# Performance work log

Hardware: AMD Instinct MI355X
Metric: run time of the kernel (lower is better)

Reference implementation:

```python
import jax, jax.numpy as jnp
import numpy as np

N_HEAD = 12
D_MODEL = 768
B, T = 1, 1024


def _rope(x):
    # x: (B, H, T, Dh). Matches torch RoPE: split even/odd, cat halves.
    Dh = x.shape[-1]
    t = x.shape[2]
    inv_freq = 1.0 / (10000.0 ** (jnp.arange(0, Dh, 2, dtype=jnp.float32) / Dh))
    freqs = jnp.arange(t, dtype=jnp.float32)[:, None] * inv_freq[None, :]  # (T, Dh/2)
    cos = jnp.cos(freqs)[None, None]  # (1,1,T,Dh/2)
    sin = jnp.sin(freqs)[None, None]
    x1 = x[..., 0::2]
    x2 = x[..., 1::2]
    return jnp.concatenate([-x2 * sin + x1 * cos, x1 * sin + x2 * cos], axis=-1)


def _wedge(x, A, id_bias):
    # S = (A - A^T) + diag(id_bias_h), per head h; x: (B,H,T,Dh)
    skew = A - A.T  # (Dh, Dh)
    S = skew[None, :, :] + jax.vmap(jnp.diag)(id_bias)  # (H, Dh, Dh)
    flow = jnp.einsum('bhtd,hde->bhte', x, S)
    return x + flow


def _forward(x, WV_w, WV_b, WK_w, WK_b, WQ_w, A, id_bias, sink, v_nulls, WO_w, WO_b):
    b, t, c = x.shape
    n_br = WO_w.shape[0]
    n_sh = n_br
    dh = c // n_br
    h_tot = n_br * n_sh
    scale = dh ** -0.5

    q = (x @ WQ_w).reshape(b, t, h_tot, dh).transpose(0, 2, 1, 3)      # (B,Htot,T,Dh)
    k_base = (x @ WK_w + WK_b).reshape(b, t, n_sh, dh).transpose(0, 2, 1, 3)
    v_base = (x @ WV_w + WV_b).reshape(b, t, n_sh, dh).transpose(0, 2, 1, 3)
    k = jnp.tile(k_base, (1, n_br, 1, 1))  # (B,Htot,T,Dh)
    v = jnp.tile(v_base, (1, n_br, 1, 1))

    q = _rope(_wedge(q, A, id_bias))
    k = _rope(_wedge(k, A, id_bias))

    scores = jnp.einsum('bhtd,bhsd->bhts', q, k) * scale  # (B,Htot,T,T)
    causal = jnp.tril(jnp.ones((t, t), dtype=bool))
    scores = jnp.where(causal[None, None], scores, -jnp.inf)

    sinks = jnp.broadcast_to(sink.reshape(1, h_tot, 1, 1), (b, h_tot, t, 1))
    probs = jax.nn.softmax(jnp.concatenate([scores, sinks], axis=-1), axis=-1)
    probs_tok, probs_sink = probs[..., :t], probs[..., t:]

    out_tok = jnp.einsum('bhts,bhsd->bhtd', probs_tok, v)
    out_sink = probs_sink * v_nulls.reshape(h_tot, dh)[None, :, None, :]
    ctx = out_tok + out_sink  # (B,Htot,T,Dh)

    ctx = ctx.reshape(b, n_br, n_sh, t, dh).transpose(0, 1, 3, 2, 4).reshape(b, n_br, t, c)
    y = jnp.einsum('bntc,ncd->bntd', ctx, WO_w) + WO_b[None, :, None, :]
    return y.mean(axis=1)  # (B,T,C)


def setup_inputs() -> dict:
    key = jax.random.key(0)
    ks = jax.random.split(key, 12)
    c = D_MODEL
    n_br = N_HEAD
    dh = c // n_br
    h_tot = n_br * n_br
    s = 0.02
    return {
        'x': jax.random.normal(ks[0], (B, T, c), dtype=jnp.float32),
        'WV_w': jax.random.normal(ks[1], (c, c), dtype=jnp.float32) * s,
        'WV_b': jnp.zeros((c,), dtype=jnp.float32),
        'WK_w': jax.random.normal(ks[2], (c, c), dtype=jnp.float32) * s,
        'WK_b': jnp.zeros((c,), dtype=jnp.float32),
        'WQ_w': jax.random.normal(ks[3], (c, c * n_br), dtype=jnp.float32) * s,
        'A': jax.random.normal(ks[4], (dh, dh), dtype=jnp.float32) * s,
        'id_bias': jax.random.normal(ks[5], (h_tot, dh), dtype=jnp.float32) * s,
        'sink': jax.random.normal(ks[6], (h_tot,), dtype=jnp.float32) * s,
        'v_nulls': jax.random.normal(ks[7], (n_br, c), dtype=jnp.float32) * s,
        'WO_w': jax.random.normal(ks[8], (n_br, c, c), dtype=jnp.float32) * (1.0 / np.sqrt(c)),
        'WO_b': jnp.zeros((n_br, c), dtype=jnp.float32),
    }


def reference(x, WV_w, WV_b, WK_w, WK_b, WQ_w, A, id_bias, sink, v_nulls, WO_w, WO_b):
    return _forward(x, WV_w, WV_b, WK_w, WK_b, WQ_w, A, id_bias, sink, v_nulls, WO_w, WO_b)
```

## Files before the change

### kernel.cpp

```cpp
#include <hip/hip_runtime.h>
#include <hip/hip_bf16.h>

#define T_SEQ   1024
#define C_MODEL 768
#define N_BR    12
#define DH      64
#define H_TOT   144
#define NQ      9216

typedef __bf16 bf16x8 __attribute__((ext_vector_type(8)));
typedef float  f32x4  __attribute__((ext_vector_type(4)));
typedef unsigned int u32x4 __attribute__((ext_vector_type(4)));
typedef unsigned short u16;

#define SM_OFF 3.0f

__device__ __forceinline__ void gload16(void* lds, const void* g)
{
    __builtin_amdgcn_global_load_lds(
        (const __attribute__((address_space(1))) void*)g,
        (__attribute__((address_space(3))) void*)lds, 16, 0, 0);
}

__device__ __forceinline__ void split1(float x, u16& h, u16& l)
{
    __bf16 bh = (__bf16)x;
    __bf16 bl = (__bf16)(x - (float)bh);
    h = __builtin_bit_cast(u16, bh);
    l = __builtin_bit_cast(u16, bl);
}

__device__ __forceinline__ u16 tobf(float x)
{
    return __builtin_bit_cast(u16, (__bf16)x);
}

__device__ __forceinline__ unsigned cvtpk(float a, float b)
{
    unsigned r;
    asm("v_cvt_pk_bf16_f32 %0, %1, %2" : "=v"(r) : "v"(a), "v"(b));
    return r;
}

__device__ __forceinline__ int swb(int row, int byteoff)
{
    return row * 128 + (byteoff ^ ((row & 7) << 4));
}

__device__ __forceinline__ bf16x8 ldsr8(const u16* p, int byteoff)
{
    return *reinterpret_cast<const bf16x8*>(reinterpret_cast<const char*>(p) + byteoff);
}

__device__ __forceinline__ void convt_body(const float* __restrict__ W,
                                           u16* __restrict__ out, int K, int N,
                                           int nx, int ky, float (*t)[33], int tid)
{
    const int n0 = nx * 32;
    const int k0 = ky * 32;
    const int tx = tid & 31;
    const int ty = tid >> 5;
    #pragma unroll
    for (int r = 0; r < 4; ++r)
        t[ty + r * 8][tx] = W[(size_t)(k0 + ty + r * 8) * N + n0 + tx];
    __syncthreads();
    #pragma unroll
    for (int r = 0; r < 4; ++r)
        out[(size_t)(n0 + ty + r * 8) * K + k0 + tx] = tobf(t[tx][ty + r * 8]);
}

__global__ __launch_bounds__(256)
void prep_kernel(const float* __restrict__ x, u16* __restrict__ xh,
                 const float* __restrict__ Amat, const float* __restrict__ id_bias,
                 u16* __restrict__ Mth, u16* __restrict__ Mtl,
                 const float* __restrict__ WO_b, float* __restrict__ mbias,
                 float* __restrict__ tab,
                 const float* __restrict__ WO_w, u16* __restrict__ wot,
                 const float* __restrict__ WK_w, const float* __restrict__ WV_w,
                 u16* __restrict__ wkvt)
{
    __shared__ float tsh[32][33];
    const int b   = blockIdx.x;
    const int tid = threadIdx.x;

    if (b < 128) {
        const int idx = b * 256 + tid;
        const int t = idx >> 5, i = idx & 31;
        const float inv = expf(-(float)i * (logf(10000.f) / 32.f));
        const float fr = (float)t * inv;
        tab[t * 64 + i]      = cosf(fr);
        tab[t * 64 + 32 + i] = sinf(fr);
    } else if (b < 272) {
        const int h = b - 128;
        const int base = tid * 16;
        #pragma unroll
        for (int i = 0; i < 16; ++i) {
            const int idx = base + i;
            const int e = idx >> 6, d = idx & 63;
            float v = Amat[d * 64 + e] - Amat[e * 64 + d];
            if (d == e) v += 1.0f + id_bias[h * 64 + d];
            u16 hh, ll;
            split1(v, hh, ll);
            Mth[(size_t)h * 4096 + idx] = hh;
            Mtl[(size_t)h * 4096 + idx] = ll;
        }
    } else if (b < 275) {
        const int d = (b - 272) * 256 + tid;
        if (d < C_MODEL) {
            float s = 0.f;
            #pragma unroll
            for (int n = 0; n < N_BR; ++n) s += WO_b[n * C_MODEL + d];
            mbias[d] = s * (1.0f / 12.0f);
        }
    } else if (b < 1043) {
        const size_t i = (size_t)(b - 275) * 1024 + tid * 4;
        float4 v = *reinterpret_cast<const float4*>(&x[i]);
        ushort4 o = { tobf(v.x), tobf(v.y), tobf(v.z), tobf(v.w) };
        *reinterpret_cast<ushort4*>(&xh[i]) = o;
    } else if (b < 7955) {
        const int u = b - 1043;
        convt_body(WO_w, wot, NQ, C_MODEL, u % 24, u / 24, tsh, tid);
    } else if (b < 8531) {
        const int u = b - 7955;
        convt_body(WK_w, wkvt, C_MODEL, C_MODEL, u % 24, u / 24, tsh, tid);
    } else {
        const int u = b - 8531;
        convt_body(WV_w, wkvt + 589824, C_MODEL, C_MODEL, u % 24, u / 24, tsh, tid);
    }
}

#define BM 128
#define BN 128
#define BK 32

__global__ __launch_bounds__(256)
void gemm_bf16_kernel(const u16* __restrict__ A, const u16* __restrict__ B,
                      float* __restrict__ Cp, int M, int N, int K)
{
    __shared__ __align__(16) u16 sA[BM * BK], sB[BN * BK];

    const int tid  = threadIdx.x;
    const int lane = tid & 63;
    const int wid  = tid >> 6;
    const int m0   = blockIdx.y * BM;
    const int n0   = blockIdx.x * BN;
    const int kc   = K / gridDim.z;
    const int kbeg = blockIdx.z * kc;
    const int kend = kbeg + kc;

    const int wm = (wid >> 1) * 64;
    const int wn = (wid & 1) * 64;

    f32x4 acc[4][4];
    #pragma unroll
    for (int i = 0; i < 4; ++i)
        #pragma unroll
        for (int j = 0; j < 4; ++j)
            #pragma unroll
            for (int r = 0; r < 4; ++r) acc[i][j][r] = 0.f;

    const int r0 = tid >> 2;
    const int c0 = tid & 3;
    const int rA = wm + (lane & 15);
    const int rB = wn + (lane & 15);
    const int co = (lane >> 4) * 8;

    for (int k0 = kbeg; k0 < kend; k0 += BK) {
        gload16(&sA[(size_t)tid * 8],         &A[(size_t)(m0 + r0)      * K + k0 + c0 * 8]);
        gload16(&sA[(size_t)(tid + 256) * 8], &A[(size_t)(m0 + r0 + 64) * K + k0 + c0 * 8]);
        gload16(&sB[(size_t)tid * 8],         &B[(size_t)(n0 + r0)      * K + k0 + c0 * 8]);
        gload16(&sB[(size_t)(tid + 256) * 8], &B[(size_t)(n0 + r0 + 64) * K + k0 + c0 * 8]);
        __syncthreads();

        bf16x8 ah[4], bh[4];
        #pragma unroll
        for (int i = 0; i < 4; ++i)
            ah[i] = *reinterpret_cast<const bf16x8*>(&sA[(size_t)(rA + i * 16) * BK + co]);
        #pragma unroll
        for (int j = 0; j < 4; ++j)
            bh[j] = *reinterpret_cast<const bf16x8*>(&sB[(size_t)(rB + j * 16) * BK + co]);
        #pragma unroll
        for (int i = 0; i < 4; ++i)
            #pragma unroll
            for (int j = 0; j < 4; ++j)
                acc[i][j] = __builtin_amdgcn_mfma_f32_16x16x32_bf16(ah[i], bh[j], acc[i][j], 0, 0, 0);
        __syncthreads();
    }

    float* Cz = Cp + (size_t)blockIdx.z * M * N;
    const int crow0 = m0 + wm + (lane >> 4) * 4;
    const int ccol0 = n0 + wn + (lane & 15);
    #pragma unroll
    for (int i = 0; i < 4; ++i)
        #pragma unroll
        for (int j = 0; j < 4; ++j)
            #pragma unroll
            for (int r = 0; r < 4; ++r)
                Cz[(size_t)(crow0 + i * 16 + r) * N + ccol0 + j * 16] = acc[i][j][r];
}

__global__ __launch_bounds__(256)
void gemm64_kernel(const u16* __restrict__ A, const u16* __restrict__ B,
                   float* __restrict__ Cp, int M, int N, int K)
{
    __shared__ __align__(16) u16 sA[64 * BK], sB[128 * BK];

    const int tid  = threadIdx.x;
    const int lane = tid & 63;
    const int wid  = tid >> 6;
    const int m0   = blockIdx.y * 64;
    const int n0   = blockIdx.x * 128;
    const int kc   = K / gridDim.z;
    const int kbeg = blockIdx.z * kc;
    const int kend = kbeg + kc;

    const int wm = (wid >> 1) * 32;
    const int wn = (wid & 1) * 64;
    const int g  = lane >> 4;
    const int li = lane & 15;

    f32x4 acc[2][4];
    #pragma unroll
    for (int i = 0; i < 2; ++i)
        #pragma unroll
        for (int j = 0; j < 4; ++j)
            #pragma unroll
            for (int r = 0; r < 4; ++r) acc[i][j][r] = 0.f;

    const int r0 = tid >> 2;
    const int c0 = (tid & 3) * 8;

    for (int k0 = kbeg; k0 < kend; k0 += BK) {
        gload16(&sA[(size_t)tid * 8],         &A[(size_t)(m0 + r0)      * K + k0 + c0]);
        gload16(&sB[(size_t)tid * 8],         &B[(size_t)(n0 + r0)      * K + k0 + c0]);
        gload16(&sB[(size_t)(tid + 256) * 8], &B[(size_t)(n0 + r0 + 64) * K + k0 + c0]);
        __syncthreads();

        bf16x8 ah[2], bh[4];
        #pragma unroll
        for (int i = 0; i < 2; ++i)
            ah[i] = *reinterpret_cast<const bf16x8*>(&sA[(size_t)(wm + 16 * i + li) * BK + g * 8]);
        #pragma unroll
        for (int j = 0; j < 4; ++j)
            bh[j] = *reinterpret_cast<const bf16x8*>(&sB[(size_t)(wn + 16 * j + li) * BK + g * 8]);
        #pragma unroll
        for (int i = 0; i < 2; ++i)
            #pragma unroll
            for (int j = 0; j < 4; ++j)
                acc[i][j] = __builtin_amdgcn_mfma_f32_16x16x32_bf16(ah[i], bh[j], acc[i][j], 0, 0, 0);
        __syncthreads();
    }

    float* Cz = Cp + (size_t)blockIdx.z * M * N;
    const int crow0 = m0 + wm + g * 4;
    const int ccol0 = n0 + wn + li;
    #pragma unroll
    for (int i = 0; i < 2; ++i)
        #pragma unroll
        for (int j = 0; j < 4; ++j)
            #pragma unroll
            for (int r = 0; r < 4; ++r)
                Cz[(size_t)(crow0 + i * 16 + r) * N + ccol0 + j * 16] = acc[i][j][r];
}

__global__ __launch_bounds__(256)
void gemm_q_rope_kernel(const u16* __restrict__ A, const u16* __restrict__ B,
                        const float* __restrict__ tab, u16* __restrict__ Q2)
{
    __shared__ __align__(16) u16 sA[64 * BK], sB[128 * BK];

    const int K = C_MODEL;
    const int tid  = threadIdx.x;
    const int lane = tid & 63;
    const int wid  = tid >> 6;
    const int m0   = blockIdx.y * 64;
    const int n0   = blockIdx.x * 128;

    const int wm = (wid >> 1) * 32;
    const int wn = (wid & 1) * 64;
    const int g  = lane >> 4;
    const int li = lane & 15;

    f32x4 acc[2][4];
    #pragma unroll
    for (int i = 0; i < 2; ++i)
        #pragma unroll
        for (int j = 0; j < 4; ++j)
            #pragma unroll
            for (int r = 0; r < 4; ++r) acc[i][j][r] = 0.f;

    const int r0 = tid >> 2;
    const int c0 = (tid & 3) * 8;

    for (int k0 = 0; k0 < K; k0 += BK) {
        gload16(&sA[(size_t)tid * 8],         &A[(size_t)(m0 + r0)      * K + k0 + c0]);
        gload16(&sB[(size_t)tid * 8],         &B[(size_t)(n0 + r0)      * K + k0 + c0]);
        gload16(&sB[(size_t)(tid + 256) * 8], &B[(size_t)(n0 + r0 + 64) * K + k0 + c0]);
        __syncthreads();

        bf16x8 ah[2], bh[4];
        #pragma unroll
        for (int i = 0; i < 2; ++i)
            ah[i] = *reinterpret_cast<const bf16x8*>(&sA[(size_t)(wm + 16 * i + li) * BK + g * 8]);
        #pragma unroll
        for (int j = 0; j < 4; ++j)
            bh[j] = *reinterpret_cast<const bf16x8*>(&sB[(size_t)(wn + 16 * j + li) * BK + g * 8]);
        #pragma unroll
        for (int i = 0; i < 2; ++i)
            #pragma unroll
            for (int j = 0; j < 4; ++j)
                acc[i][j] = __builtin_amdgcn_mfma_f32_16x16x32_bf16(ah[i], bh[j], acc[i][j], 0, 0, 0);
        __syncthreads();
    }

    const int h  = (n0 + wn) >> 6;
    const bool ev = (li & 1) == 0;
    #pragma unroll
    for (int j = 0; j < 4; ++j) {
        const int e  = j * 16 + li;
        const int i2 = e >> 1;
        #pragma unroll
        for (int i = 0; i < 2; ++i) {
            #pragma unroll
            for (int r = 0; r < 4; ++r) {
                const int t = m0 + wm + i * 16 + g * 4 + r;
                const float own = acc[i][j][r];
                const float oth = __shfl_xor(own, 1);
                const float cs = tab[t * 64 + i2];
                const float sn = tab[t * 64 + 32 + i2];
                float o; int ch;
                if (ev) { o = own * cs - oth * sn; ch = i2; }
                else    { o = oth * sn + own * cs; ch = 32 + i2; }
                Q2[((size_t)h * T_SEQ + t) * 64 + ch] = tobf(o * 0.125f);
            }
        }
    }
}

__global__ __launch_bounds__(256)
void reduce_kernel(const float* __restrict__ part, float* __restrict__ out,
                   const float* __restrict__ bias, int MN, int N, int Z, float alpha)
{
    const int i = (blockIdx.x * 256 + threadIdx.x) * 4;
    if (i >= MN) return;
    float4 s = *reinterpret_cast<const float4*>(&part[i]);
    for (int z = 1; z < Z; ++z) {
        float4 p = *reinterpret_cast<const float4*>(&part[(size_t)z * MN + i]);
        s.x += p.x; s.y += p.y; s.z += p.z; s.w += p.w;
    }
    s.x *= alpha; s.y *= alpha; s.z *= alpha; s.w *= alpha;
    if (bias) {
        const int c = i % N;
        s.x += bias[c]; s.y += bias[c + 1]; s.z += bias[c + 2]; s.w += bias[c + 3];
    }
    *reinterpret_cast<float4*>(&out[i]) = s;
}

__global__ __launch_bounds__(256)
void reduce_kv_kernel(const float* __restrict__ part, float* __restrict__ out,
                      const float* __restrict__ kb, const float* __restrict__ vb,
                      int MN, int Z)
{
    const int i = (blockIdx.x * 256 + threadIdx.x) * 4;
    if (i >= MN) return;
    float4 s = *reinterpret_cast<const float4*>(&part[i]);
    for (int z = 1; z < Z; ++z) {
        float4 p = *reinterpret_cast<const float4*>(&part[(size_t)z * MN + i]);
        s.x += p.x; s.y += p.y; s.z += p.z; s.w += p.w;
    }
    const int c = i % 1536;
    const float* bp = (c < 768) ? (kb + c) : (vb + c - 768);
    s.x += bp[0]; s.y += bp[1]; s.z += bp[2]; s.w += bp[3];
    *reinterpret_cast<float4*>(&out[i]) = s;
}

__global__ __launch_bounds__(256)
void fold_wq_kernel(const float* __restrict__ WQ, const u16* __restrict__ Mth,
                    const u16* __restrict__ Mtl, u16* __restrict__ wqt)
{
    __shared__ __align__(16) u16 sMh[4096], sMl[4096];
    __shared__ __align__(16) u16 sB[8192];

    const int h   = blockIdx.x;
    const int k0  = blockIdx.y * 128;
    const int tid = threadIdx.x;
    const int lane = tid & 63, w = tid >> 6, g = lane >> 4, li = lane & 15;

    {
        const char* gmh = (const char*)(Mth + (size_t)h * 4096);
        const char* gml = (const char*)(Mtl + (size_t)h * 4096);
        #pragma unroll
        for (int p = 0; p < 2; ++p) {
            const int u = p * 256 + tid;
            const int row = u >> 3, off = (u & 7) * 16;
            const int src = swb(row, off);
            gload16((char*)sMh + u * 16, gmh + src);
            gload16((char*)sMl + u * 16, gml + src);
        }
    }
    {
        const int r    = tid >> 1;
        const int half = tid & 1;
        const float* src = WQ + (size_t)(k0 + r) * NQ + h * 64 + half * 32;
        #pragma unroll
        for (int q = 0; q < 8; ++q) {
            float4 v = *reinterpret_cast<const float4*>(&src[q * 4]);
            ushort4 o = { tobf(v.x), tobf(v.y), tobf(v.z), tobf(v.w) };
            const int byte = swb(r, half * 64 + q * 8);
            *reinterpret_cast<ushort4*>(reinterpret_cast<char*>(sB) + byte) = o;
        }
    }
    __syncthreads();

    f32x4 acc[4][2];
    #pragma unroll
    for (int i = 0; i < 4; ++i)
        #pragma unroll
        for (int jj = 0; jj < 2; ++jj)
            #pragma unroll
            for (int r = 0; r < 4; ++r) acc[i][jj][r] = 0.f;

    bf16x8 ah[4][2], al[4][2];
    #pragma unroll
    for (int i = 0; i < 4; ++i)
        #pragma unroll
        for (int ks = 0; ks < 2; ++ks) {
            ah[i][ks] = ldsr8(sMh, swb(16 * i + li, ks * 64 + g * 16));
            al[i][ks] = ldsr8(sMl, swb(16 * i + li, ks * 64 + g * 16));
        }
    #pragma unroll
    for (int jj = 0; jj < 2; ++jj) {
        const int brow = 16 * (2 * w + jj) + li;
        #pragma unroll
        for (int ks = 0; ks < 2; ++ks) {
            bf16x8 bh = ldsr8(sB, swb(brow, ks * 64 + g * 16));
            #pragma unroll
            for (int i = 0; i < 4; ++i) {
                acc[i][jj] = __builtin_amdgcn_mfma_f32_16x16x32_bf16(ah[i][ks], bh, acc[i][jj], 0, 0, 0);
                acc[i][jj] = __builtin_amdgcn_mfma_f32_16x16x32_bf16(al[i][ks], bh, acc[i][jj], 0, 0, 0);
            }
        }
    }

    #pragma unroll
    for (int i = 0; i < 4; ++i)
        #pragma unroll
        for (int jj = 0; jj < 2; ++jj) {
            const int kc = k0 + 16 * (2 * w + jj) + li;
            #pragma unroll
            for (int r = 0; r < 4; ++r) {
                const int e = 16 * i + g * 4 + r;
                wqt[((size_t)h * 64 + e) * 768 + kc] = tobf(acc[i][jj][r]);
            }
        }
}

__global__ __launch_bounds__(256)
void wedge_mfma_kernel(const float* __restrict__ X, u16* __restrict__ Y,
                       const u16* __restrict__ Mth, const u16* __restrict__ Mtl,
                       const float* __restrict__ tab, int inStride, int headMod)
{
    const int h   = blockIdx.x;
    const int t0  = blockIdx.y * 64;
    const int tid = threadIdx.x;
    const int lane = tid & 63;
    const int w    = tid >> 6;
    const int g    = lane >> 4;
    const int li   = lane & 15;

    __shared__ __align__(16) u16 sX[4096], sMh[4096], sMl[4096];

    {
        const int r  = tid >> 2;
        const int c0 = (tid & 3) * 16;
        const float* xrow = X + (size_t)(t0 + r) * inStride + (h % headMod) * 64;
        #pragma unroll
        for (int q = 0; q < 4; ++q) {
            const int c = c0 + q * 4;
            float4 v = *reinterpret_cast<const float4*>(&xrow[c]);
            ushort4 hv = { tobf(v.x), tobf(v.y), tobf(v.z), tobf(v.w) };
            *reinterpret_cast<ushort4*>(reinterpret_cast<char*>(sX) + swb(r, 2 * c)) = hv;
        }
    }
    {
        const char* gmh = (const char*)(Mth + (size_t)h * 4096);
        const char* gml = (const char*)(Mtl + (size_t)h * 4096);
        #pragma unroll
        for (int u = 0; u < 2; ++u) {
            const int L = (u * 256 + tid) * 16;
            const int row = L >> 7, off = L & 127;
            const int src = swb(row, off);
            gload16(reinterpret_cast<char*>(sMh) + L, gmh + src);
            gload16(reinterpret_cast<char*>(sMl) + L, gml + src);
        }
    }
    __syncthreads();

    f32x4 acc[4];
    #pragma unroll
    for (int j = 0; j < 4; ++j)
        #pragma unroll
        for (int r = 0; r < 4; ++r) acc[j][r] = 0.f;

    bf16x8 ah[2];
    #pragma unroll
    for (int ks = 0; ks < 2; ++ks)
        ah[ks] = ldsr8(sX, swb(w * 16 + li, ks * 64 + g * 16));
    #pragma unroll
    for (int ks = 0; ks < 2; ++ks)
        #pragma unroll
        for (int j = 0; j < 4; ++j) {
            bf16x8 bh = ldsr8(sMh, swb(16 * j + li, ks * 64 + g * 16));
            bf16x8 bl = ldsr8(sMl, swb(16 * j + li, ks * 64 + g * 16));
            acc[j] = __builtin_amdgcn_mfma_f32_16x16x32_bf16(ah[ks], bh, acc[j], 0, 0, 0);
            acc[j] = __builtin_amdgcn_mfma_f32_16x16x32_bf16(ah[ks], bl, acc[j], 0, 0, 0);
        }

    const bool ev = (li & 1) == 0;
    #pragma unroll
    for (int j = 0; j < 4; ++j) {
        const int e = 16 * j + li;
        const int i2 = e >> 1;
        #pragma unroll
        for (int r = 0; r < 4; ++r) {
            const int t = t0 + w * 16 + g * 4 + r;
            const float own = acc[j][r];
            const float oth = __shfl_xor(own, 1);
            const float cs = tab[t * 64 + i2];
            const float sn = tab[t * 64 + 32 + i2];
            float o; int ch;
            if (ev) { o = own * cs - oth * sn; ch = i2; }
            else    { o = oth * sn + own * cs; ch = 32 + i2; }
            Y[((size_t)h * T_SEQ + t) * 64 + ch] = tobf(o);
        }
    }
}

__global__ __launch_bounds__(256)
void vt_kernel(const float* __restrict__ vb, u16* __restrict__ Vt, int stride)
{
    __shared__ float Ls[64][65];
    const int s  = blockIdx.x;
    const int t0 = blockIdx.y * 64;
    const int tid = threadIdx.x;
    {
        const int r  = tid >> 2;
        const int c0 = (tid & 3) * 16;
        const float* row = vb + (size_t)(t0 + r) * stride + s * 64;
        #pragma unroll
        for (int q = 0; q < 4; ++q) {
            float4 v = *reinterpret_cast<const float4*>(&row[c0 + q * 4]);
            Ls[r][c0 + q * 4 + 0] = v.x; Ls[r][c0 + q * 4 + 1] = v.y;
            Ls[r][c0 + q * 4 + 2] = v.z; Ls[r][c0 + q * 4 + 3] = v.w;
        }
    }
    __syncthreads();
    {
        const int d  = tid >> 2;
        const int tq = (tid & 3) * 16;
        u16* orow = Vt + ((size_t)s * 64 + d) * T_SEQ + t0 + tq;
        #pragma unroll
        for (int q = 0; q < 4; ++q) {
            ushort4 o;
            o.x = tobf(Ls[tq + q * 4 + 0][d]);
            o.y = tobf(Ls[tq + q * 4 + 1][d]);
            o.z = tobf(Ls[tq + q * 4 + 2][d]);
            o.w = tobf(Ls[tq + q * 4 + 3][d]);
            *reinterpret_cast<ushort4*>(&orow[q * 4]) = o;
        }
    }
}

__device__ __forceinline__ void attn_stage_kv(
    int buf, int kv0, int h, int s, int tid,
    const u16* __restrict__ K2, const u16* __restrict__ Vt,
    u16* sK, u16* sV)
{
    const char* gk = (const char*)(K2 + ((size_t)h * T_SEQ + kv0) * 64);
    const char* gv = (const char*)Vt + (size_t)s * 131072 + kv0 * 2;
    #pragma unroll
    for (int p = 0; p < 2; ++p) {
        const int u = p * 256 + tid;
        const int row = u >> 3;
        const int off = (u & 7) * 16;
        const int sw  = off ^ ((row & 7) << 4);
        const int j  = row >> 4, g2 = (row >> 2) & 3, rr = row & 3;
        const int srow = 32 * (j & 1) + 8 * g2 + 4 * (j >> 1) + rr;
        gload16((char*)sK + buf * 8192 + u * 16, gk + srow * 128 + sw);
        gload16((char*)sV + buf * 8192 + u * 16, gv + row * 2048 + sw);
    }
}

template<bool DIAG>
__device__ __forceinline__ void attn_tile_sw(
    int kv0, int qglob, int g, int li,
    const u16* sK, const u16* sV, const bf16x8* qa,
    f32x4* acc, float& psum)
{
    f32x4 sacc[4];
    #pragma unroll
    for (int j = 0; j < 4; ++j)
        #pragma unroll
        for (int r = 0; r < 4; ++r) sacc[j][r] = 0.f;

    __builtin_amdgcn_s_setprio(1);
    #pragma unroll
    for (int ks = 0; ks < 2; ++ks)
        #pragma unroll
        for (int j = 0; j < 4; ++j) {
            bf16x8 kb = ldsr8(sK, swb(16 * j + li, ks * 64 + g * 16));
            sacc[j] = __builtin_amdgcn_mfma_f32_16x16x32_bf16(kb, qa[ks], sacc[j], 0, 0, 0);
        }
    __builtin_amdgcn_s_setprio(0);

    float p[4][4];
    const int kvb = kv0 + 8 * g;
    #pragma unroll
    for (int j = 0; j < 4; ++j)
        #pragma unroll
        for (int r = 0; r < 4; ++r) {
            float sv_ = sacc[j][r];
            if (DIAG) {
                const int kv = kvb + 32 * (j & 1) + 4 * (j >> 1) + r;
                if (kv > qglob) sv_ = -__builtin_inff();
            }
            p[j][r] = __expf(sv_ - SM_OFF);
        }
    psum += ((p[0][0] + p[0][1]) + (p[0][2] + p[0][3]))
          + ((p[1][0] + p[1][1]) + (p[1][2] + p[1][3]))
          + ((p[2][0] + p[2][1]) + (p[2][2] + p[2][3]))
          + ((p[3][0] + p[3][1]) + (p[3][2] + p[3][3]));

    __builtin_amdgcn_s_setprio(1);
    #pragma unroll
    for (int ks = 0; ks < 2; ++ks) {
        u32x4 pw;
        pw[0] = cvtpk(p[ks][0],     p[ks][1]);
        pw[1] = cvtpk(p[ks][2],     p[ks][3]);
        pw[2] = cvtpk(p[ks + 2][0], p[ks + 2][1]);
        pw[3] = cvtpk(p[ks + 2][2], p[ks + 2][3]);
        bf16x8 pa = __builtin_bit_cast(bf16x8, pw);
        #pragma unroll
        for (int j = 0; j < 4; ++j) {
            bf16x8 vb = ldsr8(sV, swb(16 * j + li, ks * 64 + g * 16));
            acc[j] = __builtin_amdgcn_mfma_f32_16x16x32_bf16(vb, pa, acc[j], 0, 0, 0);
        }
    }
    __builtin_amdgcn_s_setprio(0);
}

__global__ __launch_bounds__(256)
void attn_mfma_kernel(const u16* __restrict__ Q2, const u16* __restrict__ K2,
                      const u16* __restrict__ Vt, const float* __restrict__ sink,
                      const float* __restrict__ v_nulls, u16* __restrict__ ctxb)
{
    const int h  = blockIdx.x;
    const int qt = 15 - (int)blockIdx.y;
    const int s  = h % N_BR;
    const int tid  = threadIdx.x;
    const int lane = tid & 63, w = tid >> 6, g = lane >> 4, li = lane & 15;

    __shared__ __align__(16) u16 sQ[4096];
    __shared__ __align__(16) u16 sK[8192];
    __shared__ __align__(16) u16 sV[8192];

    {
        const char* gq = (const char*)(Q2 + ((size_t)h * T_SEQ + qt * 64) * 64);
        #pragma unroll
        for (int p = 0; p < 2; ++p) {
            const int u = p * 256 + tid;
            const int row = u >> 3, off = (u & 7) * 16;
            gload16((char*)sQ + u * 16, gq + row * 128 + (off ^ ((row & 7) << 4)));
        }
    }
    attn_stage_kv(0, 0, h, s, tid, K2, Vt, sK, sV);
    __syncthreads();

    bf16x8 qa[2];
    #pragma unroll
    for (int ks = 0; ks < 2; ++ks)
        qa[ks] = ldsr8(sQ, swb(w * 16 + li, ks * 64 + g * 16));

    f32x4 acc[4];
    #pragma unroll
    for (int j = 0; j < 4; ++j)
        #pragma unroll
        for (int r = 0; r < 4; ++r) acc[j][r] = 0.f;
    float psum = 0.f;

    const int qglob = qt * 64 + w * 16 + li;
    const int nt = qt + 1;
    int cur = 0;
    for (int kt = 0; kt < nt - 1; ++kt) {
        attn_stage_kv(cur ^ 1, (kt + 1) * 64, h, s, tid, K2, Vt, sK, sV);
        attn_tile_sw<false>(kt * 64, qglob, g, li,
                            sK + cur * 4096, sV + cur * 4096, qa, acc, psum);
        __syncthreads();
        cur ^= 1;
    }
    attn_tile_sw<true>(qt * 64, qglob, g, li,
                       sK + cur * 4096, sV + cur * 4096, qa, acc, psum);

    psum += __shfl_xor(psum, 16);
    psum += __shfl_xor(psum, 32);
    const float es = __expf(sink[h] - SM_OFF);
    const float rz = 1.0f / (psum + es);

    const int t = qt * 64 + w * 16 + li;
    u16* orow = ctxb + (size_t)t * NQ + h * 64;
    const float* vn = v_nulls + h * 64;
    #pragma unroll
    for (int j = 0; j < 4; ++j) {
        const int d0 = 16 * j + 4 * g;
        float4 vnv = *reinterpret_cast<const float4*>(&vn[d0]);
        ushort4 o;
        o.x = tobf((acc[j][0] + es * vnv.x) * rz);
        o.y = tobf((acc[j][1] + es * vnv.y) * rz);
        o.z = tobf((acc[j][2] + es * vnv.z) * rz);
        o.w = tobf((acc[j][3] + es * vnv.w) * rz);
        *reinterpret_cast<ushort4*>(&orow[d0]) = o;
    }
}

extern "C" void kernel_launch(void* const* d_in, const int* in_sizes, int n_in,
                              void* d_out, int out_size, void* d_ws, size_t ws_size,
                              hipStream_t stream)
{
    (void)in_sizes; (void)n_in; (void)out_size; (void)ws_size;

    const float* x       = (const float*)d_in[0];
    const float* WV_w    = (const float*)d_in[1];
    const float* WV_b    = (const float*)d_in[2];
    const float* WK_w    = (const float*)d_in[3];
    const float* WK_b    = (const float*)d_in[4];
    const float* WQ_w    = (const float*)d_in[5];
    const float* Amat    = (const float*)d_in[6];
    const float* id_bias = (const float*)d_in[7];
    const float* sink    = (const float*)d_in[8];
    const float* v_nulls = (const float*)d_in[9];
    const float* WO_w    = (const float*)d_in[10];
    const float* WO_b    = (const float*)d_in[11];
    float* out = (float*)d_out;

    float* tab    = (float*)d_ws;
    float* mbias  = tab + 65536;
    float* kvbase = mbias + 768;
    u16* Mth  = (u16*)(kvbase + 1572864);
    u16* Mtl  = Mth + 589824;
    u16* xh   = Mtl + 589824;
    u16* wqt  = xh + 786432;
    u16* wkvt = wqt + 7077888;
    u16* wot  = wkvt + 1179648;
    u16* K2   = wot + 7077888;
    u16* Vt   = K2 + 9437184;
    u16* Q2   = Vt + 786432;
    u16* ctxb = Q2 + 9437184;
    float* pkv = (float*)(ctxb + 9437184);

    float* outpart = (float*)K2;

    const dim3 blk(256);

    prep_kernel<<<dim3(9107), blk, 0, stream>>>(
        x, xh, Amat, id_bias, Mth, Mtl, WO_b, mbias, tab, WO_w, wot, WK_w, WV_w, wkvt);

    fold_wq_kernel<<<dim3(H_TOT, 6), blk, 0, stream>>>(WQ_w, Mth, Mtl, wqt);

    gemm_bf16_kernel<<<dim3(12, 8, 4), blk, 0, stream>>>(
        xh, wkvt, pkv, T_SEQ, 1536, C_MODEL);
    reduce_kv_kernel<<<dim3(1536), blk, 0, stream>>>(pkv, kvbase, WK_b, WV_b, 1572864, 4);

    wedge_mfma_kernel<<<dim3(H_TOT, 16), blk, 0, stream>>>(
        kvbase, K2, Mth, Mtl, tab, 1536, N_BR);
    vt_kernel<<<dim3(12, 16), blk, 0, stream>>>(kvbase + 768, Vt, 1536);

    gemm_q_rope_kernel<<<dim3(72, 16), blk, 0, stream>>>(xh, wqt, tab, Q2);

    attn_mfma_kernel<<<dim3(H_TOT, 16), blk, 0, stream>>>(
        Q2, K2, Vt, sink, v_nulls, ctxb);

    gemm64_kernel<<<dim3(6, 16, 12), blk, 0, stream>>>(
        ctxb, wot, outpart, T_SEQ, C_MODEL, NQ);
    reduce_kernel<<<dim3(768), blk, 0, stream>>>(
        outpart, out, mbias, 786432, C_MODEL, 12, 1.0f / 12.0f);
}
```

Measured before the change: 181.2 us.

## Fold log2e into Q scale, use raw exp2, MFMA row sums, merge wedge/vt

Folds log2(e) into the Q prescale and the softmax offset so the attention inner loop can use the raw v_exp_f32 instead of __expf. Row sums of probabilities are computed with an extra MFMA against a ones vector rather than scalar adds and shuffles, so they come from the same bf16-rounded probabilities used in the PV product. Q fragments are read straight from global memory into registers instead of being staged through LDS. The wedge and V-transpose kernels are merged into one launch. The bf16-rounded row sum and the extra MFMA per tile trade a little precision and matrix-core work for fewer VALU operations.

```diff
diff --git a/kernel.cpp b/kernel.cpp
--- a/kernel.cpp
+++ b/kernel.cpp
@@ -14,6 +14,8 @@
 typedef unsigned short u16;
 
 #define SM_OFF 3.0f
+#define LOG2E  1.44269504089f
+#define QSCALE (0.125f * LOG2E)
 
 __device__ __forceinline__ void gload16(void* lds, const void* g)
 {
@@ -39,6 +41,13 @@
 {
     unsigned r;
     asm("v_cvt_pk_bf16_f32 %0, %1, %2" : "=v"(r) : "v"(a), "v"(b));
+    return r;
+}
+
+__device__ __forceinline__ float exp2raw(float x)
+{
+    float r;
+    asm("v_exp_f32 %0, %1" : "=v"(r) : "v"(x));
     return r;
 }
 
@@ -331,7 +340,7 @@
                 float o; int ch;
                 if (ev) { o = own * cs - oth * sn; ch = i2; }
                 else    { o = oth * sn + own * cs; ch = 32 + i2; }
-                Q2[((size_t)h * T_SEQ + t) * 64 + ch] = tobf(o * 0.125f);
+                Q2[((size_t)h * T_SEQ + t) * 64 + ch] = tobf(o * QSCALE);
             }
         }
     }
@@ -456,117 +465,115 @@
 }
 
 __global__ __launch_bounds__(256)
-void wedge_mfma_kernel(const float* __restrict__ X, u16* __restrict__ Y,
-                       const u16* __restrict__ Mth, const u16* __restrict__ Mtl,
-                       const float* __restrict__ tab, int inStride, int headMod)
-{
-    const int h   = blockIdx.x;
+void wedge_vt_kernel(const float* __restrict__ KV, u16* __restrict__ K2,
+                     u16* __restrict__ Vt,
+                     const u16* __restrict__ Mth, const u16* __restrict__ Mtl,
+                     const float* __restrict__ tab)
+{
+    __shared__ __align__(16) char smem[24576];
+    const int b   = blockIdx.x;
     const int t0  = blockIdx.y * 64;
     const int tid = threadIdx.x;
-    const int lane = tid & 63;
-    const int w    = tid >> 6;
-    const int g    = lane >> 4;
-    const int li   = lane & 15;
-
-    __shared__ __align__(16) u16 sX[4096], sMh[4096], sMl[4096];
-
-    {
-        const int r  = tid >> 2;
-        const int c0 = (tid & 3) * 16;
-        const float* xrow = X + (size_t)(t0 + r) * inStride + (h % headMod) * 64;
-        #pragma unroll
-        for (int q = 0; q < 4; ++q) {
-            const int c = c0 + q * 4;
-            float4 v = *reinterpret_cast<const float4*>(&xrow[c]);
-            ushort4 hv = { tobf(v.x), tobf(v.y), tobf(v.z), tobf(v.w) };
-            *reinterpret_cast<ushort4*>(reinterpret_cast<char*>(sX) + swb(r, 2 * c)) = hv;
-        }
-    }
-    {
-        const char* gmh = (const char*)(Mth + (size_t)h * 4096);
-        const char* gml = (const char*)(Mtl + (size_t)h * 4096);
-        #pragma unroll
-        for (int u = 0; u < 2; ++u) {
-            const int L = (u * 256 + tid) * 16;
-            const int row = L >> 7, off = L & 127;
-            const int src = swb(row, off);
-            gload16(reinterpret_cast<char*>(sMh) + L, gmh + src);
-            gload16(reinterpret_cast<char*>(sMl) + L, gml + src);
-        }
-    }
-    __syncthreads();
-
-    f32x4 acc[4];
-    #pragma unroll
-    for (int j = 0; j < 4; ++j)
-        #pragma unroll
-        for (int r = 0; r < 4; ++r) acc[j][r] = 0.f;
-
-    bf16x8 ah[2];
-    #pragma unroll
-    for (int ks = 0; ks < 2; ++ks)
-        ah[ks] = ldsr8(sX, swb(w * 16 + li, ks * 64 + g * 16));
-    #pragma unroll
-    for (int ks = 0; ks < 2; ++ks)
+
+    if (b < H_TOT) {
+        u16* sX  = (u16*)smem;
+        u16* sMh = (u16*)(smem + 8192);
+        u16* sMl = (u16*)(smem + 16384);
+        const int h = b;
+        const int lane = tid & 63, w = tid >> 6, g = lane >> 4, li = lane & 15;
+
+        {
+            const int r  = tid >> 2;
+            const int c0 = (tid & 3) * 16;
+            const float* xrow = KV + (size_t)(t0 + r) * 1536 + (h % N_BR) * 64;
+            #pragma unroll
+            for (int q = 0; q < 4; ++q) {
+                const int c = c0 + q * 4;
+                float4 v = *reinterpret_cast<const float4*>(&xrow[c]);
+                ushort4 hv = { tobf(v.x), tobf(v.y), tobf(v.z), tobf(v.w) };
+                *reinterpret_cast<ushort4*>((char*)sX + swb(r, 2 * c)) = hv;
+            }
+        }
+        {
+            const char* gmh = (const char*)(Mth + (size_t)h * 4096);
+            const char* gml = (const char*)(Mtl + (size_t)h * 4096);
+            #pragma unroll
+            for (int u = 0; u < 2; ++u) {
+                const int L = (u * 256 + tid) * 16;
+                const int row = L >> 7, off = L & 127;
+                const int src = swb(row, off);
+                gload16((char*)sMh + L, gmh + src);
+                gload16((char*)sMl + L, gml + src);
+            }
+        }
+        __syncthreads();
+
+        f32x4 acc[4];
+        #pragma unroll
+        for (int j = 0; j < 4; ++j)
+            #pragma unroll
+            for (int r = 0; r < 4; ++r) acc[j][r] = 0.f;
+
+        bf16x8 ah[2];
+        #pragma unroll
+        for (int ks = 0; ks < 2; ++ks)
+            ah[ks] = ldsr8(sX, swb(w * 16 + li, ks * 64 + g * 16));
+        #pragma unroll
+        for (int ks = 0; ks < 2; ++ks)
+            #pragma unroll
+            for (int j = 0; j < 4; ++j) {
+                bf16x8 bh = ldsr8(sMh, swb(16 * j + li, ks * 64 + g * 16));
+                bf16x8 bl = ldsr8(sMl, swb(16 * j + li, ks * 64 + g * 16));
+                acc[j] = __builtin_amdgcn_mfma_f32_16x16x32_bf16(ah[ks], bh, acc[j], 0, 0, 0);
+                acc[j] = __builtin_amdgcn_mfma_f32_16x16x32_bf16(ah[ks], bl, acc[j], 0, 0, 0);
+            }
+
+        const bool ev = (li & 1) == 0;
         #pragma unroll
         for (int j = 0; j < 4; ++j) {
-            bf16x8 bh = ldsr8(sMh, swb(16 * j + li, ks * 64 + g * 16));
-            bf16x8 bl = ldsr8(sMl, swb(16 * j + li, ks * 64 + g * 16));
-            acc[j] = __builtin_amdgcn_mfma_f32_16x16x32_bf16(ah[ks], bh, acc[j], 0, 0, 0);
-            acc[j] = __builtin_amdgcn_mfma_f32_16x16x32_bf16(ah[ks], bl, acc[j], 0, 0, 0);
-        }
-
-    const bool ev = (li & 1) == 0;
-    #pragma unroll
-    for (int j = 0; j < 4; ++j) {
-        const int e = 16 * j + li;
-        const int i2 = e >> 1;
-        #pragma unroll
-        for (int r = 0; r < 4; ++r) {
-            const int t = t0 + w * 16 + g * 4 + r;
-            const float own = acc[j][r];
-            const float oth = __shfl_xor(own, 1);
-            const float cs = tab[t * 64 + i2];
-            const float sn = tab[t * 64 + 32 + i2];
-            float o; int ch;
-            if (ev) { o = own * cs - oth * sn; ch = i2; }
-            else    { o = oth * sn + own * cs; ch = 32 + i2; }
-            Y[((size_t)h * T_SEQ + t) * 64 + ch] = tobf(o);
-        }
-    }
-}
-
-__global__ __launch_bounds__(256)
-void vt_kernel(const float* __restrict__ vb, u16* __restrict__ Vt, int stride)
-{
-    __shared__ float Ls[64][65];
-    const int s  = blockIdx.x;
-    const int t0 = blockIdx.y * 64;
-    const int tid = threadIdx.x;
-    {
-        const int r  = tid >> 2;
-        const int c0 = (tid & 3) * 16;
-        const float* row = vb + (size_t)(t0 + r) * stride + s * 64;
-        #pragma unroll
-        for (int q = 0; q < 4; ++q) {
-            float4 v = *reinterpret_cast<const float4*>(&row[c0 + q * 4]);
-            Ls[r][c0 + q * 4 + 0] = v.x; Ls[r][c0 + q * 4 + 1] = v.y;
-            Ls[r][c0 + q * 4 + 2] = v.z; Ls[r][c0 + q * 4 + 3] = v.w;
-        }
-    }
-    __syncthreads();
-    {
-        const int d  = tid >> 2;
-        const int tq = (tid & 3) * 16;
-        u16* orow = Vt + ((size_t)s * 64 + d) * T_SEQ + t0 + tq;
-        #pragma unroll
-        for (int q = 0; q < 4; ++q) {
-            ushort4 o;
-            o.x = tobf(Ls[tq + q * 4 + 0][d]);
-            o.y = tobf(Ls[tq + q * 4 + 1][d]);
-            o.z = tobf(Ls[tq + q * 4 + 2][d]);
-            o.w = tobf(Ls[tq + q * 4 + 3][d]);
-            *reinterpret_cast<ushort4*>(&orow[q * 4]) = o;
+            const int e = 16 * j + li;
+            const int i2 = e >> 1;
+            #pragma unroll
+            for (int r = 0; r < 4; ++r) {
+                const int t = t0 + w * 16 + g * 4 + r;
+                const float own = acc[j][r];
+                const float oth = __shfl_xor(own, 1);
+                const float cs = tab[t * 64 + i2];
+                const float sn = tab[t * 64 + 32 + i2];
+                float o; int ch;
+                if (ev) { o = own * cs - oth * sn; ch = i2; }
+                else    { o = oth * sn + own * cs; ch = 32 + i2; }
+                K2[((size_t)h * T_SEQ + t) * 64 + ch] = tobf(o);
+            }
+        }
+    } else {
+        float (*Ls)[65] = (float (*)[65])smem;
+        const int s = b - H_TOT;
+        {
+            const int r  = tid >> 2;
+            const int c0 = (tid & 3) * 16;
+            const float* row = KV + (size_t)(t0 + r) * 1536 + 768 + s * 64;
+            #pragma unroll
+            for (int q = 0; q < 4; ++q) {
+                float4 v = *reinterpret_cast<const float4*>(&row[c0 + q * 4]);
+                Ls[r][c0 + q * 4 + 0] = v.x; Ls[r][c0 + q * 4 + 1] = v.y;
+                Ls[r][c0 + q * 4 + 2] = v.z; Ls[r][c0 + q * 4 + 3] = v.w;
+            }
+        }
+        __syncthreads();
+        {
+            const int d  = tid >> 2;
+            const int tq = (tid & 3) * 16;
+            u16* orow = Vt + ((size_t)s * 64 + d) * T_SEQ + t0 + tq;
+            #pragma unroll
+            for (int q = 0; q < 4; ++q) {
+                ushort4 o;
+                o.x = tobf(Ls[tq + q * 4 + 0][d]);
+                o.y = tobf(Ls[tq + q * 4 + 1][d]);
+                o.z = tobf(Ls[tq + q * 4 + 2][d]);
+                o.w = tobf(Ls[tq + q * 4 + 3][d]);
+                *reinterpret_cast<ushort4*>(&orow[q * 4]) = o;
+            }
         }
     }
 }
@@ -594,14 +601,14 @@
 template<bool DIAG>
 __device__ __forceinline__ void attn_tile_sw(
     int kv0, int qglob, int g, int li,
-    const u16* sK, const u16* sV, const bf16x8* qa,
-    f32x4* acc, float& psum)
+    const u16* sK, const u16* sV, const bf16x8* qa, const bf16x8 ones,
+    f32x4* acc, f32x4& psacc)
 {
     f32x4 sacc[4];
     #pragma unroll
     for (int j = 0; j < 4; ++j)
         #pragma unroll
-        for (int r = 0; r < 4; ++r) sacc[j][r] = 0.f;
+        for (int r = 0; r < 4; ++r) sacc[j][r] = -SM_OFF * LOG2E;
 
     __builtin_amdgcn_s_setprio(1);
     #pragma unroll
@@ -624,12 +631,8 @@
                 const int kv = kvb + 32 * (j & 1) + 4 * (j >> 1) + r;
                 if (kv > qglob) sv_ = -__builtin_inff();
             }
-            p[j][r] = __expf(sv_ - SM_OFF);
-        }
-    psum += ((p[0][0] + p[0][1]) + (p[0][2] + p[0][3]))
-          + ((p[1][0] + p[1][1]) + (p[1][2] + p[1][3]))
-          + ((p[2][0] + p[2][1]) + (p[2][2] + p[2][3]))
-          + ((p[3][0] + p[3][1]) + (p[3][2] + p[3][3]));
+            p[j][r] = exp2raw(sv_);
+        }
 
     __builtin_amdgcn_s_setprio(1);
     #pragma unroll
@@ -640,6 +643,7 @@
         pw[2] = cvtpk(p[ks + 2][0], p[ks + 2][1]);
         pw[3] = cvtpk(p[ks + 2][2], p[ks + 2][3]);
         bf16x8 pa = __builtin_bit_cast(bf16x8, pw);
+        psacc = __builtin_amdgcn_mfma_f32_16x16x32_bf16(ones, pa, psacc, 0, 0, 0);
         #pragma unroll
         for (int j = 0; j < 4; ++j) {
             bf16x8 vb = ldsr8(sV, swb(16 * j + li, ks * 64 + g * 16));
@@ -660,33 +664,30 @@
     const int tid  = threadIdx.x;
     const int lane = tid & 63, w = tid >> 6, g = lane >> 4, li = lane & 15;
 
-    __shared__ __align__(16) u16 sQ[4096];
     __shared__ __align__(16) u16 sK[8192];
     __shared__ __align__(16) u16 sV[8192];
 
-    {
-        const char* gq = (const char*)(Q2 + ((size_t)h * T_SEQ + qt * 64) * 64);
-        #pragma unroll
-        for (int p = 0; p < 2; ++p) {
-            const int u = p * 256 + tid;
-            const int row = u >> 3, off = (u & 7) * 16;
-            gload16((char*)sQ + u * 16, gq + row * 128 + (off ^ ((row & 7) << 4)));
-        }
-    }
+    const u16* qrow = Q2 + ((size_t)h * T_SEQ + qt * 64 + w * 16 + li) * 64;
+    bf16x8 qa[2];
+    qa[0] = *reinterpret_cast<const bf16x8*>(qrow + g * 8);
+    qa[1] = *reinterpret_cast<const bf16x8*>(qrow + 32 + g * 8);
+
+    bf16x8 ones;
+    #pragma unroll
+    for (int e = 0; e < 8; ++e) ones[e] = (__bf16)1.0f;
+
     attn_stage_kv(0, 0, h, s, tid, K2, Vt, sK, sV);
+
+    f32x4 acc[4];
+    #pragma unroll
+    for (int j = 0; j < 4; ++j)
+        #pragma unroll
+        for (int r = 0; r < 4; ++r) acc[j][r] = 0.f;
+    f32x4 psacc;
+    #pragma unroll
+    for (int r = 0; r < 4; ++r) psacc[r] = 0.f;
+
     __syncthreads();
-
-    bf16x8 qa[2];
-    #pragma unroll
-    for (int ks = 0; ks < 2; ++ks)
-        qa[ks] = ldsr8(sQ, swb(w * 16 + li, ks * 64 + g * 16));
-
-    f32x4 acc[4];
-    #pragma unroll
-    for (int j = 0; j < 4; ++j)
-        #pragma unroll
-        for (int r = 0; r < 4; ++r) acc[j][r] = 0.f;
-    float psum = 0.f;
 
     const int qglob = qt * 64 + w * 16 + li;
     const int nt = qt + 1;
@@ -694,17 +695,15 @@
     for (int kt = 0; kt < nt - 1; ++kt) {
         attn_stage_kv(cur ^ 1, (kt + 1) * 64, h, s, tid, K2, Vt, sK, sV);
         attn_tile_sw<false>(kt * 64, qglob, g, li,
-                            sK + cur * 4096, sV + cur * 4096, qa, acc, psum);
+                            sK + cur * 4096, sV + cur * 4096, qa, ones, acc, psacc);
         __syncthreads();
         cur ^= 1;
     }
     attn_tile_sw<true>(qt * 64, qglob, g, li,
-                       sK + cur * 4096, sV + cur * 4096, qa, acc, psum);
-
-    psum += __shfl_xor(psum, 16);
-    psum += __shfl_xor(psum, 32);
+                       sK + cur * 4096, sV + cur * 4096, qa, ones, acc, psacc);
+
     const float es = __expf(sink[h] - SM_OFF);
-    const float rz = 1.0f / (psum + es);
+    const float rz = 1.0f / (psacc[0] + es);
 
     const int t = qt * 64 + w * 16 + li;
     u16* orow = ctxb + (size_t)t * NQ + h * 64;
@@ -770,9 +769,8 @@
         xh, wkvt, pkv, T_SEQ, 1536, C_MODEL);
     reduce_kv_kernel<<<dim3(1536), blk, 0, stream>>>(pkv, kvbase, WK_b, WV_b, 1572864, 4);
 
-    wedge_mfma_kernel<<<dim3(H_TOT, 16), blk, 0, stream>>>(
-        kvbase, K2, Mth, Mtl, tab, 1536, N_BR);
-    vt_kernel<<<dim3(12, 16), blk, 0, stream>>>(kvbase + 768, Vt, 1536);
+    wedge_vt_kernel<<<dim3(156, 16), blk, 0, stream>>>(
+        kvbase, K2, Vt, Mth, Mtl, tab);
 
     gemm_q_rope_kernel<<<dim3(72, 16), blk, 0, stream>>>(xh, wqt, tab, Q2);
 
```

Measured after the change: 177.2 us. 1.02x faster.
